# Kernel optimization log

Hardware: AMD Instinct MI355X
Metric: run time of the kernel (lower is better)

The kernel has to match this reference:

```python
import jax, jax.numpy as jnp
import numpy as np

HEADS = 8
EPS = 1e-5

def _conv2d(x, w, b):
    # x: (b,c,h,w), w: (out_c,in_c,3,3), padding=1 (SAME)
    y = jax.lax.conv_general_dilated(x, w, (1, 1), ((1, 1), (1, 1)),
                                     dimension_numbers=('NCHW', 'OIHW', 'NCHW'))
    return y + b[None, :, None, None]

def _mcl(x, cw, cb, pw):
    # MultichannelLinear: conv then per-channel pointwise matmul over the h (feature) dim
    y = _conv2d(x, cw, cb)                      # (b,c,in_f,w)
    return jnp.einsum('bchw,cfh->bcfw', y, pw)  # (b,c,out_f,w)

def _ln(x, g, b):
    # MultichannelLayerNorm over the feature (h) axis with per-channel affine
    mu = x.mean(axis=2, keepdims=True)
    var = x.var(axis=2, keepdims=True)
    xn = (x - mu) * jax.lax.rsqrt(var + EPS)
    return xn * g[None, :, :, None] + b[None, :, :, None]

def _rope(t):
    # lucidrains RotaryEmbedding.rotate_queries_or_keys, interleaved pairs; t: (...,w,d)
    d = t.shape[-1]
    w = t.shape[-2]
    inv = 1.0 / (10000.0 ** (jnp.arange(0, d, 2, dtype=jnp.float32) / d))
    ang = jnp.arange(w, dtype=jnp.float32)[:, None] * inv[None, :]   # (w, d/2)
    cos = jnp.repeat(jnp.cos(ang), 2, axis=-1)
    sin = jnp.repeat(jnp.sin(ang), 2, axis=-1)
    t2 = t.reshape(t.shape[:-1] + (d // 2, 2))
    rot = jnp.stack([-t2[..., 1], t2[..., 0]], axis=-1).reshape(t.shape)
    return t * cos + rot * sin

def _split_heads(y, nh):
    b, c, f, w = y.shape
    return y.transpose(0, 1, 3, 2).reshape(b, c, w, nh, f // nh).transpose(0, 1, 3, 2, 4)  # (b,c,nh,w,dh)

def _forward(x, embed_cw, embed_cb, embed_pw, norm1_g, norm1_b,
             q_cw, q_cb, q_pw, k_cw, k_cb, k_pw, v_cw, v_cb, v_pw,
             o_cw, o_cb, o_pw, norm2_g, norm2_b,
             ffn1_cw, ffn1_cb, ffn1_pw, ffn2_cw, ffn2_cb, ffn2_pw):
    b, c_in, hdim, w = x.shape
    h0 = _mcl(x, embed_cw, embed_cb, embed_pw)          # (b,c,feat,w)
    # --- multichannel multihead attention with inline RoPE ---
    xn = _ln(h0, norm1_g, norm1_b)
    q = _rope(_split_heads(_mcl(xn, q_cw, q_cb, q_pw), HEADS))   # (b,c,nh,w,dh)
    k = _rope(_split_heads(_mcl(xn, k_cw, k_cb, k_pw), HEADS))
    v = _split_heads(_mcl(xn, v_cw, v_cb, v_pw), HEADS)
    qk = jnp.einsum('bchqd,bchkd->bchqk', q, k) / jnp.sqrt(jnp.float32(hdim))  # scale by sqrt(h), per source
    a = jnp.einsum('bchqk,bchkd->bchqd', jax.nn.softmax(qk, axis=-1), v)
    bb, cc, nh, ww, dh = a.shape
    a = a.transpose(0, 1, 3, 2, 4).reshape(bb, cc, ww, nh * dh).transpose(0, 1, 3, 2)  # (b,c,feat,w)
    z = _mcl(a, o_cw, o_cb, o_pw)
    h = h0 + z
    # --- squared-ReLU FFN ---
    y = _mcl(_ln(h, norm2_g, norm2_b), ffn1_cw, ffn1_cb, ffn1_pw)
    y = jnp.maximum(y, 0.0) ** 2
    z = _mcl(y, ffn2_cw, ffn2_cb, ffn2_pw)
    h = h + z
    return jnp.concatenate([x, h], axis=1)  # (b, c_in+c_out, feat, w)

def setup_inputs() -> dict:
    key = jax.random.key(0)
    ks = jax.random.split(key, 32)
    C_IN, C, F, W, B, EXP = 8, 4, 1024, 512, 4, 4

    def p(k, shape, fan):
        return jax.random.normal(k, shape, dtype=jnp.float32) * (1.0 / np.sqrt(fan))

    inp = {
        'x': jax.random.normal(ks[0], (B, C_IN, F, W), dtype=jnp.float32),
        'embed_cw': p(ks[1], (C, C_IN, 3, 3), C_IN * 9), 'embed_cb': p(ks[2], (C,), C_IN * 9),
        'embed_pw': p(ks[3], (C, F, F), F),
        'norm1_g': jnp.ones((C, F), jnp.float32), 'norm1_b': jnp.zeros((C, F), jnp.float32),
        'q_cw': p(ks[4], (C, C, 3, 3), C * 9), 'q_cb': p(ks[5], (C,), C * 9), 'q_pw': p(ks[6], (C, F, F), F),
        'k_cw': p(ks[7], (C, C, 3, 3), C * 9), 'k_cb': p(ks[8], (C,), C * 9), 'k_pw': p(ks[9], (C, F, F), F),
        'v_cw': p(ks[10], (C, C, 3, 3), C * 9), 'v_cb': p(ks[11], (C,), C * 9), 'v_pw': p(ks[12], (C, F, F), F),
        'o_cw': p(ks[13], (C, C, 3, 3), C * 9), 'o_cb': p(ks[14], (C,), C * 9), 'o_pw': p(ks[15], (C, F, F), F),
        'norm2_g': jnp.ones((C, F), jnp.float32), 'norm2_b': jnp.zeros((C, F), jnp.float32),
        'ffn1_cw': p(ks[16], (C, C, 3, 3), C * 9), 'ffn1_cb': p(ks[17], (C,), C * 9),
        'ffn1_pw': p(ks[18], (C, F * EXP, F), F),
        'ffn2_cw': p(ks[19], (C, C, 3, 3), C * 9), 'ffn2_cb': p(ks[20], (C,), C * 9),
        'ffn2_pw': p(ks[21], (C, F, F * EXP), F * EXP),
    }
    return inp

def reference(x, embed_cw, embed_cb, embed_pw, norm1_g, norm1_b,
              q_cw, q_cb, q_pw, k_cw, k_cb, k_pw, v_cw, v_cb, v_pw,
              o_cw, o_cb, o_pw, norm2_g, norm2_b,
              ffn1_cw, ffn1_cb, ffn1_pw, ffn2_cw, ffn2_cb, ffn2_pw):
    return _forward(x, embed_cw, embed_cb, embed_pw, norm1_g, norm1_b,
                    q_cw, q_cb, q_pw, k_cw, k_cb, k_pw, v_cw, v_cb, v_pw,
                    o_cw, o_cb, o_pw, norm2_g, norm2_b,
                    ffn1_cw, ffn1_cb, ffn1_pw, ffn2_cw, ffn2_cb, ffn2_pw)
```

## Files before the change

kernel.cpp:

```cpp
#include <hip/hip_runtime.h>

typedef __attribute__((ext_vector_type(8))) short short8;
typedef __attribute__((ext_vector_type(4))) float f32x4;
typedef unsigned int uint;
typedef unsigned short ushort;

#define PLF 524288

__device__ __forceinline__ ushort f2bf(float f) {
  uint u = __float_as_uint(f);
  u += 0x7FFF + ((u >> 16) & 1);
  return (ushort)(u >> 16);
}
__device__ __forceinline__ float bf2f(ushort h) {
  return __uint_as_float(((uint)h) << 16);
}
__device__ __forceinline__ int swzf(int r) { return ((r & 3) ^ ((r >> 2) & 3)); }

#define GLOAD16(gp, lp)                                          \
  __builtin_amdgcn_global_load_lds(                              \
      (const __attribute__((address_space(1))) void*)(gp),       \
      (__attribute__((address_space(3))) void*)(lp), 16, 0, 0)

template <int CDT, int BETA, int RELU2, int MFAST, int BCVT, int BN>
__global__ __launch_bounds__(256) void mm_kernel(
    const void* __restrict__ Av, const void* __restrict__ Bv, void* __restrict__ Cv,
    int K, int lda, int ldb, int ldc,
    int aDiv, long long aS1, long long aS2,
    int bDiv, long long bS1, long long bS2,
    int cDiv, long long cS1, long long cS2, float alpha)
{
  constexpr int LDSB = 8192 + BN * 64;
  constexpr int MI = (BN == 128) ? 4 : 2;
  __shared__ char lds[2 * LDSB];
  const int nx = gridDim.x, ny = gridDim.y;
  const int nwg = nx * ny * (int)gridDim.z;
  const int o = ((int)blockIdx.z * ny + blockIdx.y) * nx + blockIdx.x;
  const int qd = nwg >> 3, rm = nwg & 7, xcd = o & 7, rot = o >> 3;
  const int wflat = (xcd < rm ? xcd * (qd + 1) : rm * (qd + 1) + (xcd - rm) * qd) + rot;
  int bx, by, bz;
  if (MFAST) { by = wflat % ny; int t2 = wflat / ny; bx = t2 % nx; bz = t2 / nx; }
  else       { bx = wflat % nx; int t2 = wflat / nx; by = t2 % ny; bz = t2 / ny; }
  const int tid = threadIdx.x;
  const long long aOff = (long long)(bz / aDiv) * aS1 + (long long)(bz % aDiv) * aS2;
  const long long bOff = (long long)(bz / bDiv) * bS1 + (long long)(bz % bDiv) * bS2;
  const long long cOff = (long long)(bz / cDiv) * cS1 + (long long)(bz % cDiv) * cS2;
  const int m0 = by * 128, n0 = bx * BN;
  const int lane = tid & 63, wid = tid >> 6;
  const int MOFF = (BN == 128) ? (wid >> 1) * 64 : wid * 32;
  const int NOFF = (BN == 128) ? (wid & 1) * 64 : 0;
  const int u = lane & 15, g = lane >> 4;
  const int sr0 = tid >> 2, sslot = tid & 3;
  const ushort* Ap = (const ushort*)Av + aOff;
  const ushort* Bp = (const ushort*)Bv + bOff;
  const float*  Bf = (const float*)Bv + bOff;

#define STAGE(buf, kt)                                                         \
  {                                                                            \
    _Pragma("unroll")                                                          \
    for (int half = 0; half < 2; ++half) {                                     \
      const int r = sr0 + 64 * half;                                           \
      const int ss = sslot ^ swzf(r);                                          \
      GLOAD16(Ap + (long long)(m0 + r) * lda + (kt) + ss * 8,                  \
              &lds[(buf) * LDSB] + wid * 1024 + half * 4096);                  \
    }                                                                          \
    _Pragma("unroll")                                                          \
    for (int bh = 0; bh < BN / 64; ++bh) {                                     \
      const int r = sr0 + 64 * bh;                                             \
      const int ss = sslot ^ swzf(r);                                          \
      if (BCVT == 0) {                                                         \
        GLOAD16(Bp + (long long)(n0 + r) * ldb + (kt) + ss * 8,                \
                &lds[(buf) * LDSB + 8192] + wid * 1024 + bh * 4096);           \
      } else {                                                                 \
        const float* srcB = Bf + (long long)(n0 + r) * ldb + (kt) + ss * 8;    \
        float4 x0 = *(const float4*)srcB;                                      \
        float4 x1 = *(const float4*)(srcB + 4);                                \
        short8 h;                                                              \
        h[0] = (short)f2bf(x0.x); h[1] = (short)f2bf(x0.y);                    \
        h[2] = (short)f2bf(x0.z); h[3] = (short)f2bf(x0.w);                    \
        h[4] = (short)f2bf(x1.x); h[5] = (short)f2bf(x1.y);                    \
        h[6] = (short)f2bf(x1.z); h[7] = (short)f2bf(x1.w);                    \
        *(short8*)(&lds[(buf) * LDSB + 8192] + r * 64 + sslot * 16) = h;       \
      }                                                                        \
    }                                                                          \
  }

  f32x4 acc[MI][4];
#pragma unroll
  for (int i = 0; i < MI; ++i)
#pragma unroll
    for (int j = 0; j < 4; ++j) acc[i][j] = (f32x4){0.f, 0.f, 0.f, 0.f};

  STAGE(0, 0);
  asm volatile("s_waitcnt vmcnt(0) lgkmcnt(0)" ::: "memory");
  __builtin_amdgcn_s_barrier();
  int cur = 0;
  for (int kt = 0; kt < K; kt += 32) {
    if (kt + 32 < K) STAGE(cur ^ 1, kt + 32);
    short8 af[MI], bfr[4];
#pragma unroll
    for (int mi = 0; mi < MI; ++mi) {
      const int r = MOFF + mi * 16 + u;
      af[mi] = *(const short8*)(&lds[cur * LDSB] + r * 64 + ((g ^ swzf(r)) * 16));
    }
#pragma unroll
    for (int ni = 0; ni < 4; ++ni) {
      const int r = NOFF + ni * 16 + u;
      bfr[ni] = *(const short8*)(&lds[cur * LDSB + 8192] + r * 64 + ((g ^ swzf(r)) * 16));
    }
#pragma unroll
    for (int mi = 0; mi < MI; ++mi)
#pragma unroll
      for (int ni = 0; ni < 4; ++ni)
        acc[mi][ni] = __builtin_amdgcn_mfma_f32_16x16x32_bf16(af[mi], bfr[ni], acc[mi][ni], 0, 0, 0);
    asm volatile("s_waitcnt vmcnt(0) lgkmcnt(0)" ::: "memory");
    __builtin_amdgcn_s_barrier();
    cur ^= 1;
  }
#undef STAGE

#pragma unroll
  for (int mi = 0; mi < MI; ++mi)
#pragma unroll
    for (int ni = 0; ni < 4; ++ni)
#pragma unroll
      for (int q = 0; q < 4; ++q) {
        const int row = m0 + MOFF + mi * 16 + g * 4 + q;
        const int col = n0 + NOFF + ni * 16 + u;
        float v = acc[mi][ni][q] * alpha;
        if (CDT == 0) {
          float* cp = (float*)Cv + cOff + (long long)row * ldc + col;
          if (BETA) v += *cp;
          *cp = v;
        } else {
          if (RELU2) { v = fmaxf(v, 0.f); v = v * v; }
          ((ushort*)Cv)[cOff + (long long)row * ldc + col] = f2bf(v);
        }
      }
}

__global__ __launch_bounds__(256) void fattn_kernel(
    const ushort* __restrict__ Qg, const ushort* __restrict__ Kg,
    const ushort* __restrict__ Vg, ushort* __restrict__ Og)
{
  __shared__ char lds[73728];
  const int hb = blockIdx.y, pl = hb >> 3, h = hb & 7;
  const int q0 = blockIdx.x * 64;
  const int tid = threadIdx.x, lane = tid & 63, wv = tid >> 6;
  const int u = lane & 15, g = lane >> 4;
  const ushort* Qh = Qg + (size_t)pl * PLF + h * 128;
  const ushort* Kh = Kg + (size_t)pl * PLF + h * 128;
  const ushort* Vh = Vg + (size_t)pl * PLF + (size_t)(h * 128) * 512;
  ushort* Oh = Og + (size_t)pl * PLF + h * 128;

  short8 qf[4];
  const int qrow = q0 + wv * 16 + u;
#pragma unroll
  for (int dc = 0; dc < 4; ++dc)
    qf[dc] = *(const short8*)(Qh + (size_t)qrow * 1024 + dc * 32 + g * 8);

#define STAGE_KV(buf, kt)                                                     \
  {                                                                           \
    _Pragma("unroll")                                                         \
    for (int it = 0; it < 4; ++it) {                                          \
      const int off = tid * 16 + it * 4096;                                   \
      const int krow = off >> 8, kslot = (off >> 4) & 15;                     \
      GLOAD16(Kh + (size_t)((kt) * 64 + krow) * 1024 +                        \
                  ((kslot ^ ((krow & 7) << 1)) * 8),                          \
              &lds[(buf) * 16384] + off);                                     \
      const int vrow = off >> 7, vslot = (off >> 4) & 7;                      \
      GLOAD16(Vh + (size_t)vrow * 512 + (kt) * 64 + ((vslot ^ (vrow & 7)) * 8), \
              &lds[32768 + (buf) * 16384] + off);                             \
    }                                                                         \
  }

  f32x4 oacc[8];
#pragma unroll
  for (int i = 0; i < 8; ++i) oacc[i] = (f32x4){0.f, 0.f, 0.f, 0.f};
  float m_run = -3.0e38f, l_run = 0.f;

  STAGE_KV(0, 0);
  asm volatile("s_waitcnt vmcnt(0)" ::: "memory");
  __syncthreads();
  int cur = 0;
  for (int kt = 0; kt < 8; ++kt) {
    if (kt + 1 < 8) STAGE_KV(cur ^ 1, kt + 1);
    f32x4 sacc[4];
#pragma unroll
    for (int kn = 0; kn < 4; ++kn) sacc[kn] = (f32x4){0.f, 0.f, 0.f, 0.f};
#pragma unroll
    for (int kn = 0; kn < 4; ++kn) {
      const int r = kn * 16 + u;
      const char* kb = &lds[cur * 16384] + r * 256;
#pragma unroll
      for (int dc = 0; dc < 4; ++dc) {
        short8 kf = *(const short8*)(kb + (((dc * 4 + g) ^ ((u & 7) << 1)) * 16));
        sacc[kn] = __builtin_amdgcn_mfma_f32_16x16x32_bf16(kf, qf[dc], sacc[kn], 0, 0, 0);
      }
    }
    float pm = -3.0e38f;
#pragma unroll
    for (int kn = 0; kn < 4; ++kn)
#pragma unroll
      for (int r = 0; r < 4; ++r) {
        sacc[kn][r] *= 0.03125f;
        pm = fmaxf(pm, sacc[kn][r]);
      }
    pm = fmaxf(pm, __shfl_xor(pm, 16));
    pm = fmaxf(pm, __shfl_xor(pm, 32));
    const float m_new = fmaxf(m_run, pm);
    const float es = __expf(m_run - m_new);
    float psum = 0.f;
    uint pw[4][2];
#pragma unroll
    for (int kn = 0; kn < 4; ++kn) {
      float p0 = __expf(sacc[kn][0] - m_new);
      float p1 = __expf(sacc[kn][1] - m_new);
      float p2 = __expf(sacc[kn][2] - m_new);
      float p3 = __expf(sacc[kn][3] - m_new);
      psum += (p0 + p1) + (p2 + p3);
      pw[kn][0] = (uint)f2bf(p0) | ((uint)f2bf(p1) << 16);
      pw[kn][1] = (uint)f2bf(p2) | ((uint)f2bf(p3) << 16);
    }
    psum += __shfl_xor(psum, 16);
    psum += __shfl_xor(psum, 32);
    l_run = l_run * es + psum;
    m_run = m_new;
    char* pb = &lds[65536 + wv * 2048] + u * 128 + (g & 1) * 8;
#pragma unroll
    for (int kn = 0; kn < 4; ++kn)
      *(uint2*)(pb + (((2 * kn + (g >> 1)) ^ (u & 7)) * 16)) =
          make_uint2(pw[kn][0], pw[kn][1]);
    float es_o[4];
#pragma unroll
    for (int r = 0; r < 4; ++r) es_o[r] = __shfl(es, g * 4 + r);
#pragma unroll
    for (int nd = 0; nd < 8; ++nd)
#pragma unroll
      for (int r = 0; r < 4; ++r) oacc[nd][r] *= es_o[r];
    const char* prd = &lds[65536 + wv * 2048] + u * 128;
    short8 pf[2];
#pragma unroll
    for (int kc = 0; kc < 2; ++kc)
      pf[kc] = *(const short8*)(prd + (((kc * 4 + g) ^ (u & 7)) * 16));
#pragma unroll
    for (int nd = 0; nd < 8; ++nd) {
      const int vr = nd * 16 + u;
      const char* vb = &lds[32768 + cur * 16384] + vr * 128;
#pragma unroll
      for (int kc = 0; kc < 2; ++kc) {
        short8 vf = *(const short8*)(vb + (((kc * 4 + g) ^ (u & 7)) * 16));
        oacc[nd] = __builtin_amdgcn_mfma_f32_16x16x32_bf16(pf[kc], vf, oacc[nd], 0, 0, 0);
      }
    }
    asm volatile("s_waitcnt vmcnt(0)" ::: "memory");
    __syncthreads();
    cur ^= 1;
  }
#undef STAGE_KV
  const float inv_l = 1.f / l_run;
  float inv_o[4];
#pragma unroll
  for (int r = 0; r < 4; ++r) inv_o[r] = __shfl(inv_l, g * 4 + r);
#pragma unroll
  for (int nd = 0; nd < 8; ++nd)
#pragma unroll
    for (int r = 0; r < 4; ++r) {
      const int row = q0 + wv * 16 + g * 4 + r;
      Oh[(size_t)row * 1024 + nd * 16 + u] = f2bf(oacc[nd][r] * inv_o[r]);
    }
}

__global__ __launch_bounds__(256) void cvt_kernel(
    const float4* __restrict__ s, short8* __restrict__ d)
{
  const int i = blockIdx.x * 256 + threadIdx.x;
  const float4 a = s[2 * i], b = s[2 * i + 1];
  short8 h;
  h[0] = (short)f2bf(a.x); h[1] = (short)f2bf(a.y);
  h[2] = (short)f2bf(a.z); h[3] = (short)f2bf(a.w);
  h[4] = (short)f2bf(b.x); h[5] = (short)f2bf(b.y);
  h[6] = (short)f2bf(b.z); h[7] = (short)f2bf(b.w);
  d[i] = h;
}

template <int CIN>
__global__ __launch_bounds__(256) void conv4c_kernel(
    const ushort* __restrict__ in, const float* __restrict__ wt,
    const float* __restrict__ bias, ushort* __restrict__ outp, int log2F)
{
  const int idx = blockIdx.x * 256 + threadIdx.x;
  const int F8m = (1 << (log2F - 3)) - 1;
  const int f8 = idx & F8m;
  const int w = (idx >> (log2F - 3)) & 511;
  const int bb = idx >> (log2F + 6);
  const int f0 = f8 << 3;
  float acc[4][8];
#pragma unroll
  for (int co = 0; co < 4; ++co) {
    const float bv = bias[co];
#pragma unroll
    for (int j = 0; j < 8; ++j) acc[co][j] = bv;
  }
  const bool lok = f8 > 0, rok = f8 < F8m;
#pragma unroll
  for (int ci = 0; ci < CIN; ++ci) {
    const ushort* base = in + (((size_t)(bb * CIN + ci)) << (log2F + 9));
#pragma unroll
    for (int dxw = 0; dxw < 3; ++dxw) {
      const int w2 = w + dxw - 1;
      if (w2 < 0 || w2 > 511) continue;
      const ushort* rp = base + ((size_t)w2 << log2F) + f0;
      const short8 cen = *(const short8*)rp;
      float xv[10];
      xv[0] = lok ? bf2f(rp[-1]) : 0.f;
#pragma unroll
      for (int j = 0; j < 8; ++j) xv[j + 1] = bf2f((ushort)cen[j]);
      xv[9] = rok ? bf2f(rp[8]) : 0.f;
#pragma unroll
      for (int co = 0; co < 4; ++co) {
        const float* wp = wt + (co * CIN + ci) * 9;
        const float k0 = wp[dxw], k1 = wp[3 + dxw], k2 = wp[6 + dxw];
#pragma unroll
        for (int j = 0; j < 8; ++j)
          acc[co][j] += k0 * xv[j] + k1 * xv[j + 1] + k2 * xv[j + 2];
      }
    }
  }
#pragma unroll
  for (int co = 0; co < 4; ++co) {
    short8 o;
#pragma unroll
    for (int j = 0; j < 8; ++j) o[j] = (short)f2bf(acc[co][j]);
    *(short8*)(outp + (((size_t)(bb * 4 + co)) << (log2F + 9)) + ((size_t)w << log2F) + f0) = o;
  }
}

__global__ __launch_bounds__(256) void ln_kernel(
    const float* __restrict__ H, const float* __restrict__ gam,
    const float* __restrict__ bet, ushort* __restrict__ XN)
{
  const int wid = threadIdx.x >> 6, lane = threadIdx.x & 63;
  const int row = blockIdx.x * 4 + wid;
  const int c = (row >> 9) & 3;
  const float* xp = H + (size_t)row * 1024;
  float4 v[4];
  float s = 0.f, q = 0.f;
#pragma unroll
  for (int p = 0; p < 4; ++p) {
    v[p] = *(const float4*)(xp + p * 256 + lane * 4);
    s += v[p].x + v[p].y + v[p].z + v[p].w;
    q += v[p].x * v[p].x + v[p].y * v[p].y + v[p].z * v[p].z + v[p].w * v[p].w;
  }
#pragma unroll
  for (int o = 32; o > 0; o >>= 1) { s += __shfl_xor(s, o); q += __shfl_xor(q, o); }
  const float mu = s * (1.f / 1024.f);
  const float var = q * (1.f / 1024.f) - mu * mu;
  const float rs = rsqrtf(var + 1e-5f);
  ushort* op = XN + (size_t)row * 1024;
  const float* gp = gam + c * 1024;
  const float* bp = bet + c * 1024;
#pragma unroll
  for (int p = 0; p < 4; ++p) {
    const int f = p * 256 + lane * 4;
    float4 g4 = *(const float4*)(gp + f);
    float4 b4 = *(const float4*)(bp + f);
    ushort4 o4;
    o4.x = f2bf((v[p].x - mu) * rs * g4.x + b4.x);
    o4.y = f2bf((v[p].y - mu) * rs * g4.y + b4.y);
    o4.z = f2bf((v[p].z - mu) * rs * g4.z + b4.z);
    o4.w = f2bf((v[p].w - mu) * rs * g4.w + b4.w);
    *(ushort4*)(op + f) = o4;
  }
}

__global__ __launch_bounds__(256) void rope_kernel(uint* __restrict__ B)
{
  const int idx = blockIdx.x * 256 + threadIdx.x;
  const int fp = idx & 511;
  const int w = (idx >> 9) & 511;
  const int pl = idx >> 18;
  const int j = fp & 63;
  const float inv = __expf(-(float)j * (9.210340371976184f / 64.f));
  float sn, cs;
  sincosf((float)w * inv, &sn, &cs);
  uint* p = B + ((size_t)pl << 18) + ((size_t)w << 9) + fp;
  const uint pr = *p;
  const float e = bf2f((ushort)(pr & 0xFFFF));
  const float o = bf2f((ushort)(pr >> 16));
  const float ne = e * cs - o * sn;
  const float no = o * cs + e * sn;
  *p = ((uint)f2bf(no) << 16) | (uint)f2bf(ne);
}

__global__ __launch_bounds__(256) void tin_kernel(
    const float* __restrict__ x, ushort* __restrict__ XT,
    float* __restrict__ outp, int planeOff)
{
  __shared__ float t[32][33];
  const int f0 = blockIdx.x * 32, w0 = blockIdx.y * 32;
  const int z = blockIdx.z;
  const int tx = threadIdx.x & 31, ty = threadIdx.x >> 5;
  const int gpl = planeOff + z;
  const int b = gpl >> 3, ch = gpl & 7;
  const float* src = x + (size_t)gpl * PLF;
  float* dst0 = outp + (size_t)(b * 12 + ch) * PLF;
#pragma unroll
  for (int r = 0; r < 32; r += 8) {
    const size_t off = (size_t)(f0 + r + ty) * 512 + w0 + tx;
    const float v = src[off];
    t[r + ty][tx] = v;
    dst0[off] = v;
  }
  __syncthreads();
  ushort* dst = XT + (size_t)z * PLF;
#pragma unroll
  for (int r = 0; r < 32; r += 8) dst[(size_t)(w0 + r + ty) * 1024 + f0 + tx] = f2bf(t[tx][r + ty]);
}

__global__ __launch_bounds__(256) void tout_kernel(
    const float* __restrict__ H, float* __restrict__ out, int b0)
{
  __shared__ float t[32][33];
  const int w0 = blockIdx.x * 32, f0 = blockIdx.y * 32;
  const int p = blockIdx.z;
  const int b = b0 + (p >> 2), c = p & 3;
  const int tx = threadIdx.x & 31, ty = threadIdx.x >> 5;
  const float* src = H + (size_t)p * PLF;
#pragma unroll
  for (int r = 0; r < 32; r += 8) t[r + ty][tx] = src[(size_t)(w0 + r + ty) * 1024 + f0 + tx];
  __syncthreads();
  float* dst = out + (size_t)(b * 12 + 8 + c) * PLF;
#pragma unroll
  for (int r = 0; r < 32; r += 8) dst[(size_t)(f0 + r + ty) * 512 + w0 + tx] = t[tx][r + ty];
}

extern "C" void kernel_launch(void* const* d_in, const int* in_sizes, int n_in,
                              void* d_out, int out_size, void* d_ws, size_t ws_size,
                              hipStream_t stream)
{
  const float* x        = (const float*)d_in[0];
  const float* embed_cw = (const float*)d_in[1];
  const float* embed_cb = (const float*)d_in[2];
  const float* embed_pw = (const float*)d_in[3];
  const float* n1g      = (const float*)d_in[4];
  const float* n1b      = (const float*)d_in[5];
  const float* q_cw     = (const float*)d_in[6];
  const float* q_cb     = (const float*)d_in[7];
  const float* q_pw     = (const float*)d_in[8];
  const float* k_cw     = (const float*)d_in[9];
  const float* k_cb     = (const float*)d_in[10];
  const float* k_pw     = (const float*)d_in[11];
  const float* v_cw     = (const float*)d_in[12];
  const float* v_cb     = (const float*)d_in[13];
  const float* v_pw     = (const float*)d_in[14];
  const float* o_cw     = (const float*)d_in[15];
  const float* o_cb     = (const float*)d_in[16];
  const float* o_pw     = (const float*)d_in[17];
  const float* n2g      = (const float*)d_in[18];
  const float* n2b      = (const float*)d_in[19];
  const float* f1_cw    = (const float*)d_in[20];
  const float* f1_cb    = (const float*)d_in[21];
  const float* f1_pw    = (const float*)d_in[22];
  const float* f2_cw    = (const float*)d_in[23];
  const float* f2_cb    = (const float*)d_in[24];
  const float* f2_pw    = (const float*)d_in[25];
  float* out = (float*)d_out;

  const size_t perB = 50331648ull;
  const int N = (ws_size >= 4 * perB) ? 4 : (ws_size >= 2 * perB) ? 2 : 1;
  const int nP = 4 * N;

  char* base = (char*)d_ws;
  float*  Hf = (float*)base;
  ushort* XT = (ushort*)(base + (size_t)N * 8388608);
  ushort* XN = (ushort*)((char*)XT + (size_t)N * 8388608);
  ushort* Qb = (ushort*)((char*)XN + (size_t)N * 4194304);
  ushort* CT = (ushort*)((char*)Qb + (size_t)N * 4194304);
  ushort* Kb = (ushort*)((char*)CT + (size_t)N * 4194304);
  ushort* Vb = (ushort*)((char*)Kb + (size_t)N * 4194304);
  float*  Sf = (float*)((char*)Vb + (size_t)N * 4194304);
  ushort* Pb = (ushort*)((char*)Sf + (size_t)N * 8388608);
  ushort* MID = XT;
  ushort* F2C = Kb;
  ushort* W8  = (N == 1) ? (ushort*)Sf : Pb;
  ushort* f1w = Kb;
  ushort* f2w = XT;

  const long long W1 = 1048576;
  const long long W4 = 4194304;
  const long long P4 = 4LL * PLF;
  const long long M1 = 2097152;
  const int GCc1 = N * 256;
  const int GCc4 = N * 1024;

  for (int b0 = 0; b0 < 4; b0 += N) {
    tin_kernel<<<dim3(32, 16, 8 * N), 256, 0, stream>>>(x, XT, out, b0 * 8);
    conv4c_kernel<8><<<GCc1, 256, 0, stream>>>(XT, embed_cw, embed_cb, CT, 10);
    cvt_kernel<<<2048, 256, 0, stream>>>((const float4*)embed_pw, (short8*)W8);
    mm_kernel<0, 0, 0, 0, 0, 64><<<dim3(16, 4, nP), 256, 0, stream>>>(
        CT, W8, Hf, 1024, 1024, 1024, 1024,
        N, PLF, P4, N, W1, 0, N, PLF, P4, 1.f);
    ln_kernel<<<nP * 128, 256, 0, stream>>>(Hf, n1g, n1b, XN);
    conv4c_kernel<4><<<GCc1, 256, 0, stream>>>(XN, q_cw, q_cb, CT, 10);
    cvt_kernel<<<2048, 256, 0, stream>>>((const float4*)q_pw, (short8*)W8);
    mm_kernel<1, 0, 0, 0, 0, 64><<<dim3(16, 4, nP), 256, 0, stream>>>(
        CT, W8, Qb, 1024, 1024, 1024, 1024,
        N, PLF, P4, N, W1, 0, N, PLF, P4, 1.f);
    conv4c_kernel<4><<<GCc1, 256, 0, stream>>>(XN, k_cw, k_cb, CT, 10);
    cvt_kernel<<<2048, 256, 0, stream>>>((const float4*)k_pw, (short8*)W8);
    mm_kernel<1, 0, 0, 0, 0, 64><<<dim3(16, 4, nP), 256, 0, stream>>>(
        CT, W8, Kb, 1024, 1024, 1024, 1024,
        N, PLF, P4, N, W1, 0, N, PLF, P4, 1.f);
    conv4c_kernel<4><<<GCc1, 256, 0, stream>>>(XN, v_cw, v_cb, CT, 10);
    cvt_kernel<<<2048, 256, 0, stream>>>((const float4*)v_pw, (short8*)W8);
    mm_kernel<1, 0, 0, 0, 0, 64><<<dim3(8, 8, nP), 256, 0, stream>>>(
        W8, CT, Vb, 1024, 1024, 1024, 512,
        N, W1, 0, N, PLF, P4, N, PLF, P4, 1.f);
    rope_kernel<<<nP * 1024, 256, 0, stream>>>((uint*)Qb);
    rope_kernel<<<nP * 1024, 256, 0, stream>>>((uint*)Kb);
    fattn_kernel<<<dim3(8, nP * 8), 256, 0, stream>>>(Qb, Kb, Vb, Qb);
    conv4c_kernel<4><<<GCc1, 256, 0, stream>>>(Qb, o_cw, o_cb, CT, 10);
    cvt_kernel<<<2048, 256, 0, stream>>>((const float4*)o_pw, (short8*)W8);
    mm_kernel<0, 1, 0, 0, 0, 64><<<dim3(16, 4, nP), 256, 0, stream>>>(
        CT, W8, Hf, 1024, 1024, 1024, 1024,
        N, PLF, P4, N, W1, 0, N, PLF, P4, 1.f);
    ln_kernel<<<nP * 128, 256, 0, stream>>>(Hf, n2g, n2b, XN);
    conv4c_kernel<4><<<GCc1, 256, 0, stream>>>(XN, f1_cw, f1_cb, CT, 10);
    if (N >= 2) {
      cvt_kernel<<<8192, 256, 0, stream>>>((const float4*)f1_pw, (short8*)f1w);
      mm_kernel<1, 0, 1, 1, 0, 128><<<dim3(32, 4, nP), 256, 0, stream>>>(
          CT, f1w, MID, 1024, 1024, 1024, 4096,
          N, PLF, P4, N, W4, 0, N, M1, 4 * M1, 1.f);
    } else {
      mm_kernel<1, 0, 1, 1, 1, 128><<<dim3(32, 4, nP), 256, 0, stream>>>(
          CT, f1_pw, MID, 1024, 1024, 1024, 4096,
          N, PLF, P4, N, W4, 0, N, M1, 4 * M1, 1.f);
    }
    conv4c_kernel<4><<<GCc4, 256, 0, stream>>>(MID, f2_cw, f2_cb, F2C, 12);
    if (N >= 2) {
      cvt_kernel<<<8192, 256, 0, stream>>>((const float4*)f2_pw, (short8*)f2w);
      mm_kernel<0, 1, 0, 0, 0, 64><<<dim3(16, 4, nP), 256, 0, stream>>>(
          F2C, f2w, Hf, 4096, 4096, 4096, 1024,
          N, M1, 4 * M1, N, W4, 0, N, PLF, P4, 1.f);
    } else {
      mm_kernel<0, 1, 0, 0, 1, 128><<<dim3(8, 4, nP), 256, 0, stream>>>(
          F2C, f2_pw, Hf, 4096, 4096, 4096, 1024,
          N, M1, 4 * M1, N, W4, 0, N, PLF, P4, 1.f);
    }
    tout_kernel<<<dim3(16, 32, nP), 256, 0, stream>>>(Hf, out, b0);
  }
}
```

Measured before the change: 731.6 us.

## Fuse QKV convs, batch Q/K GEMMs, fold RoPE into GEMM epilogue, unify 128x128 tiles

Replaces three separate conv passes for Q, K and V with one conv12c kernel that reads the normalized input once and writes all twelve output channels. Q and K projections run as one batched GEMM launch (for N>=2). RoPE is applied in the GEMM epilogue through a lane shuffle, which removes the two standalone rope kernels. The mm_kernel is fixed to a 128x128 tile for every call, and buffer aliasing and the batch-stride parameters are reorganized. This cuts global memory round trips and launches, at the cost of higher register pressure in the fused conv and fewer workgroups for the smaller GEMMs.

```diff
diff --git a/kernel.cpp b/kernel.cpp
--- a/kernel.cpp
+++ b/kernel.cpp
@@ -22,17 +22,15 @@
       (const __attribute__((address_space(1))) void*)(gp),       \
       (__attribute__((address_space(3))) void*)(lp), 16, 0, 0)
 
-template <int CDT, int BETA, int RELU2, int MFAST, int BCVT, int BN>
+template <int CDT, int BETA, int RELU2, int MFAST, int BCVT, int ROPE>
 __global__ __launch_bounds__(256) void mm_kernel(
     const void* __restrict__ Av, const void* __restrict__ Bv, void* __restrict__ Cv,
     int K, int lda, int ldb, int ldc,
-    int aDiv, long long aS1, long long aS2,
-    int bDiv, long long bS1, long long bS2,
-    int cDiv, long long cS1, long long cS2, float alpha)
-{
-  constexpr int LDSB = 8192 + BN * 64;
-  constexpr int MI = (BN == 128) ? 4 : 2;
-  __shared__ char lds[2 * LDSB];
+    int aDiv, int aMod, long long aS1, long long aS2,
+    int bDiv, int bMod, long long bS1, long long bS2,
+    int cDiv, int cMod, long long cS1, long long cS2, float alpha)
+{
+  __shared__ char lds[32768];
   const int nx = gridDim.x, ny = gridDim.y;
   const int nwg = nx * ny * (int)gridDim.z;
   const int o = ((int)blockIdx.z * ny + blockIdx.y) * nx + blockIdx.x;
@@ -42,13 +40,12 @@
   if (MFAST) { by = wflat % ny; int t2 = wflat / ny; bx = t2 % nx; bz = t2 / nx; }
   else       { bx = wflat % nx; int t2 = wflat / nx; by = t2 % ny; bz = t2 / ny; }
   const int tid = threadIdx.x;
-  const long long aOff = (long long)(bz / aDiv) * aS1 + (long long)(bz % aDiv) * aS2;
-  const long long bOff = (long long)(bz / bDiv) * bS1 + (long long)(bz % bDiv) * bS2;
-  const long long cOff = (long long)(bz / cDiv) * cS1 + (long long)(bz % cDiv) * cS2;
-  const int m0 = by * 128, n0 = bx * BN;
+  const long long aOff = (long long)(bz / aDiv) * aS1 + (long long)(bz % aMod) * aS2;
+  const long long bOff = (long long)(bz / bDiv) * bS1 + (long long)(bz % bMod) * bS2;
+  const long long cOff = (long long)(bz / cDiv) * cS1 + (long long)(bz % cMod) * cS2;
+  const int m0 = by * 128, n0 = bx * 128;
   const int lane = tid & 63, wid = tid >> 6;
-  const int MOFF = (BN == 128) ? (wid >> 1) * 64 : wid * 32;
-  const int NOFF = (BN == 128) ? (wid & 1) * 64 : 0;
+  const int MOFF = (wid >> 1) * 64, NOFF = (wid & 1) * 64;
   const int u = lane & 15, g = lane >> 4;
   const int sr0 = tid >> 2, sslot = tid & 3;
   const ushort* Ap = (const ushort*)Av + aOff;
@@ -62,15 +59,10 @@
       const int r = sr0 + 64 * half;                                           \
       const int ss = sslot ^ swzf(r);                                          \
       GLOAD16(Ap + (long long)(m0 + r) * lda + (kt) + ss * 8,                  \
-              &lds[(buf) * LDSB] + wid * 1024 + half * 4096);                  \
-    }                                                                          \
-    _Pragma("unroll")                                                          \
-    for (int bh = 0; bh < BN / 64; ++bh) {                                     \
-      const int r = sr0 + 64 * bh;                                             \
-      const int ss = sslot ^ swzf(r);                                          \
+              &lds[(buf) * 16384] + wid * 1024 + half * 4096);                 \
       if (BCVT == 0) {                                                         \
         GLOAD16(Bp + (long long)(n0 + r) * ldb + (kt) + ss * 8,                \
-                &lds[(buf) * LDSB + 8192] + wid * 1024 + bh * 4096);           \
+                &lds[(buf) * 16384 + 8192] + wid * 1024 + half * 4096);        \
       } else {                                                                 \
         const float* srcB = Bf + (long long)(n0 + r) * ldb + (kt) + ss * 8;    \
         float4 x0 = *(const float4*)srcB;                                      \
@@ -80,14 +72,14 @@
         h[2] = (short)f2bf(x0.z); h[3] = (short)f2bf(x0.w);                    \
         h[4] = (short)f2bf(x1.x); h[5] = (short)f2bf(x1.y);                    \
         h[6] = (short)f2bf(x1.z); h[7] = (short)f2bf(x1.w);                    \
-        *(short8*)(&lds[(buf) * LDSB + 8192] + r * 64 + sslot * 16) = h;       \
+        *(short8*)(&lds[(buf) * 16384 + 8192] + r * 64 + sslot * 16) = h;      \
       }                                                                        \
     }                                                                          \
   }
 
-  f32x4 acc[MI][4];
-#pragma unroll
-  for (int i = 0; i < MI; ++i)
+  f32x4 acc[4][4];
+#pragma unroll
+  for (int i = 0; i < 4; ++i)
 #pragma unroll
     for (int j = 0; j < 4; ++j) acc[i][j] = (f32x4){0.f, 0.f, 0.f, 0.f};
 
@@ -97,19 +89,19 @@
   int cur = 0;
   for (int kt = 0; kt < K; kt += 32) {
     if (kt + 32 < K) STAGE(cur ^ 1, kt + 32);
-    short8 af[MI], bfr[4];
-#pragma unroll
-    for (int mi = 0; mi < MI; ++mi) {
+    short8 af[4], bfr[4];
+#pragma unroll
+    for (int mi = 0; mi < 4; ++mi) {
       const int r = MOFF + mi * 16 + u;
-      af[mi] = *(const short8*)(&lds[cur * LDSB] + r * 64 + ((g ^ swzf(r)) * 16));
+      af[mi] = *(const short8*)(&lds[cur * 16384] + r * 64 + ((g ^ swzf(r)) * 16));
     }
 #pragma unroll
     for (int ni = 0; ni < 4; ++ni) {
       const int r = NOFF + ni * 16 + u;
-      bfr[ni] = *(const short8*)(&lds[cur * LDSB + 8192] + r * 64 + ((g ^ swzf(r)) * 16));
-    }
-#pragma unroll
-    for (int mi = 0; mi < MI; ++mi)
+      bfr[ni] = *(const short8*)(&lds[cur * 16384 + 8192] + r * 64 + ((g ^ swzf(r)) * 16));
+    }
+#pragma unroll
+    for (int mi = 0; mi < 4; ++mi)
 #pragma unroll
       for (int ni = 0; ni < 4; ++ni)
         acc[mi][ni] = __builtin_amdgcn_mfma_f32_16x16x32_bf16(af[mi], bfr[ni], acc[mi][ni], 0, 0, 0);
@@ -120,7 +112,7 @@
 #undef STAGE
 
 #pragma unroll
-  for (int mi = 0; mi < MI; ++mi)
+  for (int mi = 0; mi < 4; ++mi)
 #pragma unroll
     for (int ni = 0; ni < 4; ++ni)
 #pragma unroll
@@ -133,6 +125,14 @@
           if (BETA) v += *cp;
           *cp = v;
         } else {
+          if (ROPE) {
+            const int j = (col & 127) >> 1;
+            const float infr = __expf((float)j * (-9.210340371976184f / 64.f));
+            float sn, cs;
+            __sincosf((float)row * infr, &sn, &cs);
+            const float part = __shfl_xor(v, 1);
+            v = (col & 1) ? fmaf(part, sn, v * cs) : fmaf(-part, sn, v * cs);
+          }
           if (RELU2) { v = fmaxf(v, 0.f); v = v * v; }
           ((ushort*)Cv)[cOff + (long long)row * ldc + col] = f2bf(v);
         }
@@ -336,6 +336,66 @@
   }
 }
 
+__global__ __launch_bounds__(256) void conv12c_kernel(
+    const ushort* __restrict__ in,
+    const float* __restrict__ wq, const float* __restrict__ wk, const float* __restrict__ wv,
+    const float* __restrict__ bq, const float* __restrict__ bk, const float* __restrict__ bv,
+    ushort* __restrict__ outp, int nPl)
+{
+  const int idx = blockIdx.x * 256 + threadIdx.x;
+  const int f8 = idx & 127;
+  const int w = (idx >> 7) & 511;
+  const int bb = idx >> 16;
+  const int f0 = f8 << 3;
+  const float* wsel[3] = {wq, wk, wv};
+  float acc[12][8];
+#pragma unroll
+  for (int co = 0; co < 4; ++co) {
+    const float b0 = bq[co], b1 = bk[co], b2 = bv[co];
+#pragma unroll
+    for (int j = 0; j < 8; ++j) {
+      acc[co][j] = b0; acc[4 + co][j] = b1; acc[8 + co][j] = b2;
+    }
+  }
+  const bool lok = f8 > 0, rok = f8 < 127;
+#pragma unroll
+  for (int ci = 0; ci < 4; ++ci) {
+    const ushort* base = in + (((size_t)(bb * 4 + ci)) << 19);
+#pragma unroll
+    for (int dxw = 0; dxw < 3; ++dxw) {
+      const int w2 = w + dxw - 1;
+      if (w2 < 0 || w2 > 511) continue;
+      const ushort* rp = base + ((size_t)w2 << 10) + f0;
+      const short8 cen = *(const short8*)rp;
+      float xv[10];
+      xv[0] = lok ? bf2f(rp[-1]) : 0.f;
+#pragma unroll
+      for (int j = 0; j < 8; ++j) xv[j + 1] = bf2f((ushort)cen[j]);
+      xv[9] = rok ? bf2f(rp[8]) : 0.f;
+#pragma unroll
+      for (int pj = 0; pj < 3; ++pj)
+#pragma unroll
+        for (int co = 0; co < 4; ++co) {
+          const float* wp = wsel[pj] + (co * 4 + ci) * 9;
+          const float k0 = wp[dxw], k1 = wp[3 + dxw], k2 = wp[6 + dxw];
+#pragma unroll
+          for (int j = 0; j < 8; ++j)
+            acc[pj * 4 + co][j] += k0 * xv[j] + k1 * xv[j + 1] + k2 * xv[j + 2];
+        }
+    }
+  }
+#pragma unroll
+  for (int pj = 0; pj < 3; ++pj)
+#pragma unroll
+    for (int co = 0; co < 4; ++co) {
+      short8 o;
+#pragma unroll
+      for (int j = 0; j < 8; ++j) o[j] = (short)f2bf(acc[pj * 4 + co][j]);
+      *(short8*)(outp + (((size_t)(pj * nPl + bb * 4 + co)) << 19) +
+                 ((size_t)w << 10) + f0) = o;
+    }
+}
+
 __global__ __launch_bounds__(256) void ln_kernel(
     const float* __restrict__ H, const float* __restrict__ gam,
     const float* __restrict__ bet, ushort* __restrict__ XN)
@@ -372,25 +432,6 @@
     o4.w = f2bf((v[p].w - mu) * rs * g4.w + b4.w);
     *(ushort4*)(op + f) = o4;
   }
-}
-
-__global__ __launch_bounds__(256) void rope_kernel(uint* __restrict__ B)
-{
-  const int idx = blockIdx.x * 256 + threadIdx.x;
-  const int fp = idx & 511;
-  const int w = (idx >> 9) & 511;
-  const int pl = idx >> 18;
-  const int j = fp & 63;
-  const float inv = __expf(-(float)j * (9.210340371976184f / 64.f));
-  float sn, cs;
-  sincosf((float)w * inv, &sn, &cs);
-  uint* p = B + ((size_t)pl << 18) + ((size_t)w << 9) + fp;
-  const uint pr = *p;
-  const float e = bf2f((ushort)(pr & 0xFFFF));
-  const float o = bf2f((ushort)(pr >> 16));
-  const float ne = e * cs - o * sn;
-  const float no = o * cs + e * sn;
-  *p = ((uint)f2bf(no) << 16) | (uint)f2bf(ne);
 }
 
 __global__ __launch_bounds__(256) void tin_kernel(
@@ -476,21 +517,22 @@
   ushort* XT = (ushort*)(base + (size_t)N * 8388608);
   ushort* XN = (ushort*)((char*)XT + (size_t)N * 8388608);
   ushort* Qb = (ushort*)((char*)XN + (size_t)N * 4194304);
-  ushort* CT = (ushort*)((char*)Qb + (size_t)N * 4194304);
-  ushort* Kb = (ushort*)((char*)CT + (size_t)N * 4194304);
-  ushort* Vb = (ushort*)((char*)Kb + (size_t)N * 4194304);
-  float*  Sf = (float*)((char*)Vb + (size_t)N * 4194304);
-  ushort* Pb = (ushort*)((char*)Sf + (size_t)N * 8388608);
+  ushort* Kb = (ushort*)((char*)Qb + (size_t)N * 4194304);
+  ushort* CT = (ushort*)((char*)Kb + (size_t)N * 4194304);
+  ushort* Vb = (ushort*)((char*)CT + (size_t)N * 4194304);
+  ushort* SfPb = (ushort*)((char*)Vb + (size_t)N * 4194304);
+  ushort* CT3 = SfPb;
+  ushort* W8  = SfPb;
+  ushort* WQK = XT;
   ushort* MID = XT;
-  ushort* F2C = Kb;
-  ushort* W8  = (N == 1) ? (ushort*)Sf : Pb;
-  ushort* f1w = Kb;
+  ushort* f1w = Vb;
+  ushort* F2C = Vb;
   ushort* f2w = XT;
 
   const long long W1 = 1048576;
   const long long W4 = 4194304;
-  const long long P4 = 4LL * PLF;
   const long long M1 = 2097152;
+  const long long CH3 = (long long)nP * PLF;
   const int GCc1 = N * 256;
   const int GCc4 = N * 1024;
 
@@ -498,55 +540,58 @@
     tin_kernel<<<dim3(32, 16, 8 * N), 256, 0, stream>>>(x, XT, out, b0 * 8);
     conv4c_kernel<8><<<GCc1, 256, 0, stream>>>(XT, embed_cw, embed_cb, CT, 10);
     cvt_kernel<<<2048, 256, 0, stream>>>((const float4*)embed_pw, (short8*)W8);
-    mm_kernel<0, 0, 0, 0, 0, 64><<<dim3(16, 4, nP), 256, 0, stream>>>(
+    mm_kernel<0, 0, 0, 0, 0, 0><<<dim3(8, 4, nP), 256, 0, stream>>>(
         CT, W8, Hf, 1024, 1024, 1024, 1024,
-        N, PLF, P4, N, W1, 0, N, PLF, P4, 1.f);
+        1, 1, PLF, 0, 4, 4, 0, W1, 1, 1, PLF, 0, 1.f);
     ln_kernel<<<nP * 128, 256, 0, stream>>>(Hf, n1g, n1b, XN);
-    conv4c_kernel<4><<<GCc1, 256, 0, stream>>>(XN, q_cw, q_cb, CT, 10);
-    cvt_kernel<<<2048, 256, 0, stream>>>((const float4*)q_pw, (short8*)W8);
-    mm_kernel<1, 0, 0, 0, 0, 64><<<dim3(16, 4, nP), 256, 0, stream>>>(
-        CT, W8, Qb, 1024, 1024, 1024, 1024,
-        N, PLF, P4, N, W1, 0, N, PLF, P4, 1.f);
-    conv4c_kernel<4><<<GCc1, 256, 0, stream>>>(XN, k_cw, k_cb, CT, 10);
-    cvt_kernel<<<2048, 256, 0, stream>>>((const float4*)k_pw, (short8*)W8);
-    mm_kernel<1, 0, 0, 0, 0, 64><<<dim3(16, 4, nP), 256, 0, stream>>>(
-        CT, W8, Kb, 1024, 1024, 1024, 1024,
-        N, PLF, P4, N, W1, 0, N, PLF, P4, 1.f);
-    conv4c_kernel<4><<<GCc1, 256, 0, stream>>>(XN, v_cw, v_cb, CT, 10);
+    conv12c_kernel<<<GCc1, 256, 0, stream>>>(XN, q_cw, k_cw, v_cw,
+                                             q_cb, k_cb, v_cb, CT3, nP);
+    if (N >= 2) {
+      cvt_kernel<<<2048, 256, 0, stream>>>((const float4*)q_pw, (short8*)WQK);
+      cvt_kernel<<<2048, 256, 0, stream>>>((const float4*)k_pw, (short8*)(WQK) + 524288);
+      mm_kernel<1, 0, 0, 0, 0, 1><<<dim3(8, 4, 2 * nP), 256, 0, stream>>>(
+          CT3, WQK, Qb, 1024, 1024, 1024, 1024,
+          1, 1, PLF, 0, nP, 4, 4 * W1, W1, 1, 1, PLF, 0, 1.f);
+    } else {
+      mm_kernel<1, 0, 0, 0, 1, 1><<<dim3(8, 4, nP), 256, 0, stream>>>(
+          CT3, q_pw, Qb, 1024, 1024, 1024, 1024,
+          1, 1, PLF, 0, 4, 4, 0, W1, 1, 1, PLF, 0, 1.f);
+      mm_kernel<1, 0, 0, 0, 1, 1><<<dim3(8, 4, nP), 256, 0, stream>>>(
+          CT3 + CH3, k_pw, Kb, 1024, 1024, 1024, 1024,
+          1, 1, PLF, 0, 4, 4, 0, W1, 1, 1, PLF, 0, 1.f);
+    }
     cvt_kernel<<<2048, 256, 0, stream>>>((const float4*)v_pw, (short8*)W8);
-    mm_kernel<1, 0, 0, 0, 0, 64><<<dim3(8, 8, nP), 256, 0, stream>>>(
-        W8, CT, Vb, 1024, 1024, 1024, 512,
-        N, W1, 0, N, PLF, P4, N, PLF, P4, 1.f);
-    rope_kernel<<<nP * 1024, 256, 0, stream>>>((uint*)Qb);
-    rope_kernel<<<nP * 1024, 256, 0, stream>>>((uint*)Kb);
+    mm_kernel<1, 0, 0, 0, 0, 0><<<dim3(4, 8, nP), 256, 0, stream>>>(
+        W8, CT3 + 2 * CH3, Vb, 1024, 1024, 1024, 512,
+        4, 4, 0, W1, 1, 1, PLF, 0, 1, 1, PLF, 0, 1.f);
     fattn_kernel<<<dim3(8, nP * 8), 256, 0, stream>>>(Qb, Kb, Vb, Qb);
     conv4c_kernel<4><<<GCc1, 256, 0, stream>>>(Qb, o_cw, o_cb, CT, 10);
     cvt_kernel<<<2048, 256, 0, stream>>>((const float4*)o_pw, (short8*)W8);
-    mm_kernel<0, 1, 0, 0, 0, 64><<<dim3(16, 4, nP), 256, 0, stream>>>(
+    mm_kernel<0, 1, 0, 0, 0, 0><<<dim3(8, 4, nP), 256, 0, stream>>>(
         CT, W8, Hf, 1024, 1024, 1024, 1024,
-        N, PLF, P4, N, W1, 0, N, PLF, P4, 1.f);
+        1, 1, PLF, 0, 4, 4, 0, W1, 1, 1, PLF, 0, 1.f);
     ln_kernel<<<nP * 128, 256, 0, stream>>>(Hf, n2g, n2b, XN);
     conv4c_kernel<4><<<GCc1, 256, 0, stream>>>(XN, f1_cw, f1_cb, CT, 10);
     if (N >= 2) {
       cvt_kernel<<<8192, 256, 0, stream>>>((const float4*)f1_pw, (short8*)f1w);
-      mm_kernel<1, 0, 1, 1, 0, 128><<<dim3(32, 4, nP), 256, 0, stream>>>(
+      mm_kernel<1, 0, 1, 1, 0, 0><<<dim3(32, 4, nP), 256, 0, stream>>>(
           CT, f1w, MID, 1024, 1024, 1024, 4096,
-          N, PLF, P4, N, W4, 0, N, M1, 4 * M1, 1.f);
+          1, 1, PLF, 0, 4, 4, 0, W4, 1, 1, M1, 0, 1.f);
     } else {
-      mm_kernel<1, 0, 1, 1, 1, 128><<<dim3(32, 4, nP), 256, 0, stream>>>(
+      mm_kernel<1, 0, 1, 1, 1, 0><<<dim3(32, 4, nP), 256, 0, stream>>>(
           CT, f1_pw, MID, 1024, 1024, 1024, 4096,
-          N, PLF, P4, N, W4, 0, N, M1, 4 * M1, 1.f);
+          1, 1, PLF, 0, 4, 4, 0, W4, 1, 1, M1, 0, 1.f);
     }
     conv4c_kernel<4><<<GCc4, 256, 0, stream>>>(MID, f2_cw, f2_cb, F2C, 12);
     if (N >= 2) {
       cvt_kernel<<<8192, 256, 0, stream>>>((const float4*)f2_pw, (short8*)f2w);
-      mm_kernel<0, 1, 0, 0, 0, 64><<<dim3(16, 4, nP), 256, 0, stream>>>(
+      mm_kernel<0, 1, 0, 0, 0, 0><<<dim3(8, 4, nP), 256, 0, stream>>>(
           F2C, f2w, Hf, 4096, 4096, 4096, 1024,
-          N, M1, 4 * M1, N, W4, 0, N, PLF, P4, 1.f);
+          1, 1, M1, 0, 4, 4, 0, W4, 1, 1, PLF, 0, 1.f);
     } else {
-      mm_kernel<0, 1, 0, 0, 1, 128><<<dim3(8, 4, nP), 256, 0, stream>>>(
+      mm_kernel<0, 1, 0, 0, 1, 0><<<dim3(8, 4, nP), 256, 0, stream>>>(
           F2C, f2_pw, Hf, 4096, 4096, 4096, 1024,
-          N, M1, 4 * M1, N, W4, 0, N, PLF, P4, 1.f);
+          1, 1, M1, 0, 4, 4, 0, W4, 1, 1, PLF, 0, 1.f);
     }
     tout_kernel<<<dim3(16, 32, nP), 256, 0, stream>>>(Hf, out, b0);
   }
```

Measured after the change: 674.1 us. 1.09x faster.
